# Kernel optimization log

Measured on AMD Instinct MI355X. Metric: run time of the kernel, lower is better.

Reference implementation:

```python
import jax, jax.numpy as jnp
import numpy as np

N_NODES = 20000
N_EDGES = 320000
IN_F = 256
HID = 64
OUT_F = 64
EDGE_F = 16
HEADS = 4
NUM_CLASSES = 10
NUM_GRAPHS = 40
ALPHA = 0.2  # LeakyReLU negative slope


def _xavier(key, shape):
    fan_in, fan_out = shape[0], shape[-1]
    std = 1.414 * np.sqrt(2.0 / (fan_in + fan_out))
    return jax.random.normal(key, shape, dtype=jnp.float32) * std


def setup_inputs() -> dict:
    key = jax.random.key(0)
    ks = jax.random.split(key, 12)
    x = jax.random.normal(ks[0], (N_NODES, IN_F), dtype=jnp.float32)
    edge_index = jax.random.randint(ks[1], (2, N_EDGES), 0, N_NODES, dtype=jnp.int32)
    edge_attr = jax.random.uniform(ks[2], (N_EDGES, EDGE_F), dtype=jnp.float32)
    batch = jnp.sort(jax.random.randint(ks[3], (N_NODES,), 0, NUM_GRAPHS, dtype=jnp.int32))
    # layer 0: in=IN_F, heads=HEADS, out=HID, concat
    W0 = _xavier(ks[4], (IN_F, HEADS * HID))
    a0 = _xavier(ks[5], (HEADS, 2 * HID + EDGE_F))
    # layer 1: in=HID*HEADS, heads=HEADS, out=HID, concat
    W1 = _xavier(ks[6], (HID * HEADS, HEADS * HID))
    a1 = _xavier(ks[7], (HEADS, 2 * HID + EDGE_F))
    # layer 2: in=HID*HEADS, heads=1, out=OUT_F, mean over heads
    W2 = _xavier(ks[8], (HID * HEADS, 1 * OUT_F))
    a2 = _xavier(ks[9], (1, 2 * OUT_F + EDGE_F))
    cls_w = _xavier(ks[10], (OUT_F, NUM_CLASSES))
    cls_b = jnp.zeros((NUM_CLASSES,), dtype=jnp.float32)
    return {"x": x, "edge_index": edge_index, "edge_attr": edge_attr, "batch": batch,
            "W0": W0, "a0": a0, "W1": W1, "a1": a1, "W2": W2, "a2": a2,
            "cls_w": cls_w, "cls_b": cls_b}


def gat_layer(h, W, a, edge_index, edge_attr, heads, out_f, concat):
    n = h.shape[0]
    Wh = (h @ W).reshape(n, heads, out_f)              # [N,H,D]
    src, dst = edge_index[0], edge_index[1]
    a_i, a_j, a_e = a[:, :out_f], a[:, out_f:2 * out_f], a[:, 2 * out_f:]
    # per-node head scores, gathered per edge (equivalent to concat + dot with a)
    s_i = jnp.einsum('nhd,hd->nh', Wh, a_i)            # [N,H]
    s_j = jnp.einsum('nhd,hd->nh', Wh, a_j)            # [N,H]
    s_e = edge_attr @ a_e.T                            # [E,H]
    e = s_i[src] + s_j[dst] + s_e                      # [E,H]
    e = jnp.where(e > 0, e, ALPHA * e)                 # LeakyReLU
    # NB: faithful to source — softmax over the HEADS dim (dim=1), not per-node
    att = jax.nn.softmax(e, axis=1)                    # [E,H]
    msg = att[:, :, None] * Wh[dst]                    # [E,H,D]
    h_prime = jax.ops.segment_sum(msg, src, num_segments=n)  # scatter-add to src
    if concat:
        return jax.nn.elu(h_prime.reshape(n, heads * out_f))
    return h_prime.mean(axis=1)


def reference(x, edge_index, edge_attr, batch, W0, a0, W1, a1, W2, a2, cls_w, cls_b):
    h = gat_layer(x, W0, a0, edge_index, edge_attr, HEADS, HID, True)
    h = gat_layer(h, W1, a1, edge_index, edge_attr, HEADS, HID, True)
    h = gat_layer(h, W2, a2, edge_index, edge_attr, 1, OUT_F, False)
    # global mean pool over graphs
    sums = jax.ops.segment_sum(h, batch, num_segments=NUM_GRAPHS)
    cnts = jax.ops.segment_sum(jnp.ones((h.shape[0],), h.dtype), batch, num_segments=NUM_GRAPHS)
    pooled = sums / jnp.maximum(cnts, 1.0)[:, None]
    logits = pooled @ cls_w + cls_b
    return jax.nn.log_softmax(logits, axis=1)
```

## Files before the change

kernel.cpp:

```cpp
#include <hip/hip_runtime.h>
#include <hip/hip_bf16.h>
#include <math.h>

#define N_NODES 20000
#define N_EDGES 320000
#define IN_F 256
#define HID 64
#define HEADS 4
#define OUT_F 64
#define EDGE_F 16
#define NUM_CLASSES 10
#define NUM_GRAPHS 40
#define LRELU_ALPHA 0.2f

typedef short bf16x8 __attribute__((ext_vector_type(8)));
typedef unsigned short u16x8 __attribute__((ext_vector_type(8)));
typedef float f32x4 __attribute__((ext_vector_type(4)));

static __device__ __forceinline__ float bf2f(unsigned short u) {
    union { unsigned int i; float f; } v; v.i = ((unsigned int)u) << 16; return v.f;
}
static __device__ __forceinline__ unsigned short f2bf(float f) {
    union { float f; unsigned int i; } v; v.f = f;
    unsigned int r = v.i + 0x7FFF + ((v.i >> 16) & 1);
    return (unsigned short)(r >> 16);
}
static __device__ __forceinline__ float eluf(float a) {
    return a > 0.f ? a : __expf(a) - 1.0f;
}

__global__ void prep_kernel(const float* __restrict__ W0, const float* __restrict__ W1,
                            const float* __restrict__ W2, unsigned short* __restrict__ W0b,
                            unsigned short* __restrict__ W1b, unsigned short* __restrict__ W2b,
                            int* __restrict__ cnt) {
    int b = blockIdx.x;
    if (b < 144) {
        int i = b * 256 + threadIdx.x;
        const float* src; unsigned short* dst; int off;
        if (i < 16384)      { src = W0; dst = W0b; off = i; }
        else if (i < 32768) { src = W1; dst = W1b; off = i - 16384; }
        else                { src = W2; dst = W2b; off = i - 32768; }
        float4 v = ((const float4*)src)[off];
        ushort4 o;
        o.x = f2bf(v.x); o.y = f2bf(v.y); o.z = f2bf(v.z); o.w = f2bf(v.w);
        ((ushort4*)dst)[off] = o;
    } else {
        int j = (b - 144) * 256 + threadIdx.x;
        if (j < N_NODES / 4) ((int4*)cnt)[j] = make_int4(0, 0, 0, 0);
    }
}

__global__ void count_kernel(const int4* __restrict__ src4, int* __restrict__ cnt) {
    int i = blockIdx.x * blockDim.x + threadIdx.x;
    if (i < N_EDGES / 4) {
        int4 s = src4[i];
        atomicAdd(&cnt[s.x], 1);
        atomicAdd(&cnt[s.y], 1);
        atomicAdd(&cnt[s.z], 1);
        atomicAdd(&cnt[s.w], 1);
    }
}

__global__ __launch_bounds__(1024) void scan_kernel(const int* __restrict__ cnt,
                                                    int* __restrict__ row_ptr,
                                                    int* __restrict__ cursor) {
    __shared__ int wsum[16];
    __shared__ int carry_s;
    int t = threadIdx.x;
    int lane = t & 63, wave = t >> 6;
    if (t == 0) { carry_s = 0; row_ptr[0] = 0; }
    __syncthreads();
    for (int base = 0; base < N_NODES; base += 1024) {
        int idx = base + t;
        int x0 = (idx < N_NODES) ? cnt[idx] : 0;
        int x = x0;
#pragma unroll
        for (int off = 1; off < 64; off <<= 1) {
            int y = __shfl_up(x, off, 64);
            if (lane >= off) x += y;
        }
        if (lane == 63) wsum[wave] = x;
        __syncthreads();
        if (wave == 0 && lane < 16) {
            int s = wsum[lane];
#pragma unroll
            for (int off = 1; off < 16; off <<= 1) {
                int y = __shfl_up(s, off, 64);
                if (lane >= off) s += y;
            }
            wsum[lane] = s;
        }
        __syncthreads();
        int waveoff = (wave > 0) ? wsum[wave - 1] : 0;
        int carry = carry_s;
        if (idx < N_NODES) {
            int incl = x + waveoff + carry;
            row_ptr[idx + 1] = incl;
            cursor[idx] = incl - x0;
        }
        __syncthreads();
        if (t == 0) carry_s = carry + wsum[15];
        __syncthreads();
    }
}

__global__ void scatter_kernel(const int* __restrict__ src, const int* __restrict__ dst,
                               const float* __restrict__ ea, const float* __restrict__ a0,
                               const float* __restrict__ a1, int* __restrict__ cursor,
                               int* __restrict__ srcp, int* __restrict__ dstp,
                               float* __restrict__ se01) {
    __shared__ float ae[2][4][16];
    int tid = threadIdx.x;
    if (tid < 64) ae[0][tid >> 4][tid & 15] = a0[(tid >> 4) * 144 + 128 + (tid & 15)];
    else if (tid < 128) { int t = tid - 64; ae[1][t >> 4][t & 15] = a1[(t >> 4) * 144 + 128 + (t & 15)]; }
    __syncthreads();
    int e = blockIdx.x * blockDim.x + tid;
    if (e >= N_EDGES) return;
    int s = src[e];
    int pos = atomicAdd(&cursor[s], 1);
    srcp[pos] = s;
    dstp[pos] = dst[e];
    float x[16];
#pragma unroll
    for (int k = 0; k < 16; k += 4) {
        float4 v = *(const float4*)(ea + (size_t)e * 16 + k);
        x[k] = v.x; x[k + 1] = v.y; x[k + 2] = v.z; x[k + 3] = v.w;
    }
    float4 o0 = make_float4(0.f, 0.f, 0.f, 0.f), o1 = o0;
#pragma unroll
    for (int k = 0; k < 16; ++k) {
        o0.x += x[k] * ae[0][0][k]; o0.y += x[k] * ae[0][1][k];
        o0.z += x[k] * ae[0][2][k]; o0.w += x[k] * ae[0][3][k];
        o1.x += x[k] * ae[1][0][k]; o1.y += x[k] * ae[1][1][k];
        o1.z += x[k] * ae[1][2][k]; o1.w += x[k] * ae[1][3][k];
    }
    ((float4*)se01)[(size_t)pos * 2]     = o0;
    ((float4*)se01)[(size_t)pos * 2 + 1] = o1;
}

template <bool AF32, bool SCORES>
__global__ __launch_bounds__(256) void gemm_bf16(const void* __restrict__ Aptr,
                                                 const unsigned short* __restrict__ B,
                                                 unsigned short* __restrict__ C,
                                                 const float* __restrict__ avec,
                                                 float* __restrict__ si, float* __restrict__ sj,
                                                 int M, int N, int K) {
    __shared__ unsigned short As[128][40];
    __shared__ unsigned short Bs[64][40];
    __shared__ unsigned short Cs[128][72];
    __shared__ float sa[128];
    int tid = threadIdx.x;
    if (SCORES && tid < 128) sa[tid] = avec[blockIdx.y * 144 + tid];
    int bm = blockIdx.x * 128, bn = blockIdx.y * 64;
    int w = tid >> 6, l = tid & 63;
    int wr = w * 32;
    int lr = l & 15, lk = (l >> 4) * 8;
    f32x4 acc[2][4] = {};
    int ar = tid >> 1, akc = (tid & 1) * 16;
    int bk = tid >> 3, bn8 = tid & 7, bnc = bn8 * 8;

    for (int k0 = 0; k0 < K; k0 += 32) {
        bf16x8 av0 = {}, av1 = {};
        if (bm + ar < M) {
            if constexpr (AF32) {
                const float* Af = (const float*)Aptr + (size_t)(bm + ar) * K + k0 + akc;
                float4 f0 = ((const float4*)Af)[0];
                float4 f1 = ((const float4*)Af)[1];
                float4 f2 = ((const float4*)Af)[2];
                float4 f3 = ((const float4*)Af)[3];
                av0[0] = (short)f2bf(f0.x); av0[1] = (short)f2bf(f0.y);
                av0[2] = (short)f2bf(f0.z); av0[3] = (short)f2bf(f0.w);
                av0[4] = (short)f2bf(f1.x); av0[5] = (short)f2bf(f1.y);
                av0[6] = (short)f2bf(f1.z); av0[7] = (short)f2bf(f1.w);
                av1[0] = (short)f2bf(f2.x); av1[1] = (short)f2bf(f2.y);
                av1[2] = (short)f2bf(f2.z); av1[3] = (short)f2bf(f2.w);
                av1[4] = (short)f2bf(f3.x); av1[5] = (short)f2bf(f3.y);
                av1[6] = (short)f2bf(f3.z); av1[7] = (short)f2bf(f3.w);
            } else {
                const unsigned short* Ab = (const unsigned short*)Aptr + (size_t)(bm + ar) * K + k0 + akc;
                av0 = *(const bf16x8*)Ab;
                av1 = *(const bf16x8*)(Ab + 8);
            }
        }
        *(bf16x8*)&As[ar][akc] = av0;
        *(bf16x8*)&As[ar][akc + 8] = av1;
        bf16x8 bv = *(const bf16x8*)(B + (size_t)(k0 + bk) * N + bn + bnc);
#pragma unroll
        for (int j = 0; j < 8; ++j) {
            int jj = (j + bn8) & 7;
            Bs[bnc + jj][bk] = (unsigned short)bv[jj];
        }
        __syncthreads();
        bf16x8 a0 = *(const bf16x8*)&As[wr + lr][lk];
        bf16x8 a1 = *(const bf16x8*)&As[wr + 16 + lr][lk];
        bf16x8 b0 = *(const bf16x8*)&Bs[lr][lk];
        bf16x8 b1 = *(const bf16x8*)&Bs[16 + lr][lk];
        bf16x8 b2 = *(const bf16x8*)&Bs[32 + lr][lk];
        bf16x8 b3 = *(const bf16x8*)&Bs[48 + lr][lk];
        acc[0][0] = __builtin_amdgcn_mfma_f32_16x16x32_bf16(a0, b0, acc[0][0], 0, 0, 0);
        acc[0][1] = __builtin_amdgcn_mfma_f32_16x16x32_bf16(a0, b1, acc[0][1], 0, 0, 0);
        acc[0][2] = __builtin_amdgcn_mfma_f32_16x16x32_bf16(a0, b2, acc[0][2], 0, 0, 0);
        acc[0][3] = __builtin_amdgcn_mfma_f32_16x16x32_bf16(a0, b3, acc[0][3], 0, 0, 0);
        acc[1][0] = __builtin_amdgcn_mfma_f32_16x16x32_bf16(a1, b0, acc[1][0], 0, 0, 0);
        acc[1][1] = __builtin_amdgcn_mfma_f32_16x16x32_bf16(a1, b1, acc[1][1], 0, 0, 0);
        acc[1][2] = __builtin_amdgcn_mfma_f32_16x16x32_bf16(a1, b2, acc[1][2], 0, 0, 0);
        acc[1][3] = __builtin_amdgcn_mfma_f32_16x16x32_bf16(a1, b3, acc[1][3], 0, 0, 0);
        __syncthreads();
    }
#pragma unroll
    for (int i = 0; i < 2; ++i)
#pragma unroll
        for (int j = 0; j < 4; ++j)
#pragma unroll
            for (int r = 0; r < 4; ++r)
                Cs[wr + i * 16 + (l >> 4) * 4 + r][j * 16 + (l & 15)] = f2bf(acc[i][j][r]);
    __syncthreads();
    {
        int row = tid >> 3, cc = (tid & 7) * 8;
#pragma unroll
        for (int p = 0; p < 4; ++p, row += 32) {
            if (bm + row < M) {
                bf16x8 o = *(const bf16x8*)&Cs[row][cc];
                *(bf16x8*)(C + (size_t)(bm + row) * N + bn + cc) = o;
            }
        }
    }
    if (SCORES) {
        int r = tid >> 1, half = tid & 1;
        float s0 = 0.f, s1 = 0.f;
#pragma unroll
        for (int k = 0; k < 32; ++k) {
            float f = bf2f(Cs[r][half * 32 + k]);
            s0 += f * sa[half * 32 + k];
            s1 += f * sa[64 + half * 32 + k];
        }
        s0 += __shfl_xor(s0, 1, 64);
        s1 += __shfl_xor(s1, 1, 64);
        if (half == 0 && bm + r < M) {
            si[(size_t)(bm + r) * 4 + blockIdx.y] = s0;
            sj[(size_t)(bm + r) * 4 + blockIdx.y] = s1;
        }
    }
}

__global__ void att_kernel(const int* __restrict__ srcp, const int* __restrict__ dstp,
                           const float4* __restrict__ sev, const float* __restrict__ si,
                           const float* __restrict__ sj, float4* __restrict__ attp) {
    int i = blockIdx.x * blockDim.x + threadIdx.x;
    if (i >= N_EDGES) return;
    int s = srcp[i], u = dstp[i];
    float4 siv = ((const float4*)si)[s];
    float4 sjv = ((const float4*)sj)[u];
    float4 se4 = sev[(size_t)i * 2];
    float t0 = siv.x + sjv.x + se4.x;
    float t1 = siv.y + sjv.y + se4.y;
    float t2 = siv.z + sjv.z + se4.z;
    float t3 = siv.w + sjv.w + se4.w;
    t0 = t0 > 0.f ? t0 : LRELU_ALPHA * t0;
    t1 = t1 > 0.f ? t1 : LRELU_ALPHA * t1;
    t2 = t2 > 0.f ? t2 : LRELU_ALPHA * t2;
    t3 = t3 > 0.f ? t3 : LRELU_ALPHA * t3;
    float m = fmaxf(fmaxf(t0, t1), fmaxf(t2, t3));
    float p0 = __expf(t0 - m), p1 = __expf(t1 - m), p2 = __expf(t2 - m), p3 = __expf(t3 - m);
    float inv = 1.0f / (p0 + p1 + p2 + p3);
    attp[i] = make_float4(p0 * inv, p1 * inv, p2 * inv, p3 * inv);
}

__global__ __launch_bounds__(256) void edge_agg_concat(
    const unsigned short* __restrict__ Whb, const float4* __restrict__ attp,
    const int* __restrict__ row_ptr, const int* __restrict__ dstp,
    unsigned short* __restrict__ out) {
    int v = blockIdx.x * 4 + (threadIdx.x >> 6);
    if (v >= N_NODES) return;
    int l = threadIdx.x & 63;
    int slot = l >> 4, p = l & 15;
    int beg = row_ptr[v], end = row_ptr[v + 1];
    float acc0[8] = {}, acc1[8] = {};
    int i = beg + slot;
    int u_n = 0;
    float4 at_n = make_float4(0.f, 0.f, 0.f, 0.f);
    if (i < end) { u_n = dstp[i]; at_n = attp[i]; }
    for (; i < end; i += 4) {
        int u = u_n;
        float4 at4 = at_n;
        if (i + 4 < end) { u_n = dstp[i + 4]; at_n = attp[i + 4]; }
        const unsigned short* row = Whb + (size_t)u * 256;
        u16x8 w0 = *(const u16x8*)(row + p * 8);
        u16x8 w1 = *(const u16x8*)(row + 128 + p * 8);
        float atA = (p & 8) ? at4.y : at4.x;
        float atB = (p & 8) ? at4.w : at4.z;
#pragma unroll
        for (int j = 0; j < 8; ++j) acc0[j] += atA * bf2f(w0[j]);
#pragma unroll
        for (int j = 0; j < 8; ++j) acc1[j] += atB * bf2f(w1[j]);
    }
#pragma unroll
    for (int j = 0; j < 8; ++j) {
        acc0[j] += __shfl_xor(acc0[j], 16, 64);
        acc0[j] += __shfl_xor(acc0[j], 32, 64);
        acc1[j] += __shfl_xor(acc1[j], 16, 64);
        acc1[j] += __shfl_xor(acc1[j], 32, 64);
    }
    if (slot == 0) {
        u16x8 o0, o1;
#pragma unroll
        for (int j = 0; j < 8; ++j) {
            o0[j] = f2bf(eluf(acc0[j]));
            o1[j] = f2bf(eluf(acc1[j]));
        }
        *(u16x8*)(out + (size_t)v * 256 + p * 8) = o0;
        *(u16x8*)(out + (size_t)v * 256 + 128 + p * 8) = o1;
    }
}

__global__ __launch_bounds__(256) void edge_agg_single(
    const unsigned short* __restrict__ Whb, const int* __restrict__ row_ptr,
    const int* __restrict__ dstp, float* __restrict__ out) {
    int v = blockIdx.x * 4 + (threadIdx.x >> 6);
    if (v >= N_NODES) return;
    int l = threadIdx.x & 63;
    int slot = l >> 3, p = l & 7;
    int beg = row_ptr[v], end = row_ptr[v + 1];
    float acc[8] = {};
    int i = beg + slot;
    int u_n = 0;
    if (i < end) u_n = dstp[i];
    for (; i < end; i += 8) {
        int u = u_n;
        if (i + 8 < end) u_n = dstp[i + 8];
        u16x8 w = *(const u16x8*)(Whb + (size_t)u * 64 + p * 8);
#pragma unroll
        for (int j = 0; j < 8; ++j) acc[j] += bf2f(w[j]);
    }
#pragma unroll
    for (int j = 0; j < 8; ++j) {
        acc[j] += __shfl_xor(acc[j], 8, 64);
        acc[j] += __shfl_xor(acc[j], 16, 64);
        acc[j] += __shfl_xor(acc[j], 32, 64);
    }
    if (l < 8) {
        float4 o0 = make_float4(acc[0], acc[1], acc[2], acc[3]);
        float4 o1 = make_float4(acc[4], acc[5], acc[6], acc[7]);
        *(float4*)(out + (size_t)v * 64 + p * 8) = o0;
        *(float4*)(out + (size_t)v * 64 + p * 8 + 4) = o1;
    }
}

__global__ __launch_bounds__(1024) void pool_kernel(const float* __restrict__ h3,
                                                    const int* __restrict__ batch,
                                                    float* __restrict__ pooled) {
    int g = blockIdx.x;
    int lane = threadIdx.x & 63;
    int wave = threadIdx.x >> 6;
    int lo = 0, hi = N_NODES;
    while (lo < hi) { int mid = (lo + hi) >> 1; if (batch[mid] < g) lo = mid + 1; else hi = mid; }
    int start = lo;
    lo = start; hi = N_NODES;
    while (lo < hi) { int mid = (lo + hi) >> 1; if (batch[mid] < g + 1) lo = mid + 1; else hi = mid; }
    int endi = lo;
    float s = 0.f;
    for (int v = start + wave; v < endi; v += 16) s += h3[(size_t)v * 64 + lane];
    __shared__ float red[16][64];
    red[wave][lane] = s;
    __syncthreads();
    if (wave == 0) {
        float t = red[0][lane];
#pragma unroll
        for (int w = 1; w < 16; ++w) t += red[w][lane];
        float c = (float)((endi - start) > 1 ? (endi - start) : 1);
        pooled[g * 64 + lane] = t / c;
    }
}

__global__ void classify_kernel(const float* __restrict__ pooled, const float* __restrict__ cw,
                                const float* __restrict__ cb, float* __restrict__ out) {
    int g = threadIdx.x;
    if (g >= NUM_GRAPHS) return;
    float lg[NUM_CLASSES];
#pragma unroll
    for (int c = 0; c < NUM_CLASSES; ++c) lg[c] = cb[c];
    for (int d = 0; d < OUT_F; ++d) {
        float p = pooled[g * 64 + d];
#pragma unroll
        for (int c = 0; c < NUM_CLASSES; ++c) lg[c] += p * cw[d * NUM_CLASSES + c];
    }
    float m = lg[0];
#pragma unroll
    for (int c = 1; c < NUM_CLASSES; ++c) m = fmaxf(m, lg[c]);
    float s = 0.f;
#pragma unroll
    for (int c = 0; c < NUM_CLASSES; ++c) s += expf(lg[c] - m);
    float lse = m + logf(s);
#pragma unroll
    for (int c = 0; c < NUM_CLASSES; ++c) out[g * NUM_CLASSES + c] = lg[c] - lse;
}

extern "C" void kernel_launch(void* const* d_in, const int* in_sizes, int n_in,
                              void* d_out, int out_size, void* d_ws, size_t ws_size,
                              hipStream_t stream) {
    const float* x   = (const float*)d_in[0];
    const int*   ei  = (const int*)d_in[1];
    const float* ea  = (const float*)d_in[2];
    const int* batch = (const int*)d_in[3];
    const float* W0  = (const float*)d_in[4];
    const float* a0  = (const float*)d_in[5];
    const float* W1  = (const float*)d_in[6];
    const float* a1  = (const float*)d_in[7];
    const float* W2  = (const float*)d_in[8];
    const float* cw  = (const float*)d_in[10];
    const float* cb  = (const float*)d_in[11];
    float* out = (float*)d_out;

    const int* srcg = ei;
    const int* dstg = ei + N_EDGES;

    char* ws = (char*)d_ws;
    size_t off = 0;
    auto alloc = [&](size_t bytes) -> char* {
        char* p = ws + off;
        off += (bytes + 255) & ~(size_t)255;
        return p;
    };
    unsigned short* W0b  = (unsigned short*)alloc(256 * 256 * 2);
    unsigned short* W1b  = (unsigned short*)alloc(256 * 256 * 2);
    unsigned short* W2b  = (unsigned short*)alloc(256 * 64 * 2);
    unsigned short* Whb  = (unsigned short*)alloc((size_t)N_NODES * 256 * 2);
    unsigned short* hAb  = (unsigned short*)alloc((size_t)N_NODES * 256 * 2);
    unsigned short* hBb  = (unsigned short*)alloc((size_t)N_NODES * 256 * 2);
    unsigned short* Wh2b = (unsigned short*)alloc((size_t)N_NODES * 64 * 2);
    float* si   = (float*)alloc((size_t)N_NODES * HEADS * 4);
    float* sj   = (float*)alloc((size_t)N_NODES * HEADS * 4);
    float* se01 = (float*)alloc((size_t)N_EDGES * 8 * 4);
    float* attp = (float*)alloc((size_t)N_EDGES * HEADS * 4);
    int* row_ptr = (int*)alloc((N_NODES + 1) * 4);
    int* cursor  = (int*)alloc(N_NODES * 4);
    int* cnt  = (int*)alloc(N_NODES * 4);
    int* srcp = (int*)alloc(N_EDGES * 4);
    int* dstp = (int*)alloc(N_EDGES * 4);
    float* h3 = (float*)alloc((size_t)N_NODES * 64 * 4);
    float* pooled = (float*)alloc(NUM_GRAPHS * 64 * 4);

    prep_kernel<<<144 + (N_NODES / 4 + 255) / 256, 256, 0, stream>>>(W0, W1, W2, W0b, W1b, W2b, cnt);

    count_kernel<<<(N_EDGES / 4 + 255) / 256, 256, 0, stream>>>((const int4*)srcg, cnt);
    scan_kernel<<<1, 1024, 0, stream>>>(cnt, row_ptr, cursor);
    scatter_kernel<<<(N_EDGES + 255) / 256, 256, 0, stream>>>(srcg, dstg, ea, a0, a1, cursor,
                                                              srcp, dstp, se01);

    dim3 ggrid((N_NODES + 127) / 128, 4);
    dim3 ggrid2((N_NODES + 127) / 128, 1);
    int atb = (N_EDGES + 255) / 256;
    int agb = (N_NODES + 3) / 4;

    gemm_bf16<true, true><<<ggrid, 256, 0, stream>>>(x, W0b, Whb, a0, si, sj, N_NODES, 256, 256);
    att_kernel<<<atb, 256, 0, stream>>>(srcp, dstp, (const float4*)se01, si, sj, (float4*)attp);
    edge_agg_concat<<<agb, 256, 0, stream>>>(Whb, (const float4*)attp, row_ptr, dstp, hAb);

    gemm_bf16<false, true><<<ggrid, 256, 0, stream>>>(hAb, W1b, Whb, a1, si, sj, N_NODES, 256, 256);
    att_kernel<<<atb, 256, 0, stream>>>(srcp, dstp, (const float4*)se01 + 1, si, sj, (float4*)attp);
    edge_agg_concat<<<agb, 256, 0, stream>>>(Whb, (const float4*)attp, row_ptr, dstp, hBb);

    gemm_bf16<false, false><<<ggrid2, 256, 0, stream>>>(hBb, W2b, Wh2b, nullptr, nullptr, nullptr,
                                                        N_NODES, 64, 256);
    edge_agg_single<<<agb, 256, 0, stream>>>(Wh2b, row_ptr, dstp, h3);

    pool_kernel<<<NUM_GRAPHS, 1024, 0, stream>>>(h3, batch, pooled);
    classify_kernel<<<1, 64, 0, stream>>>(pooled, cw, cb, out);
}
```

Baseline: 205.8 us.

## Recompute edge-attr scores in attention kernel instead of precomputing in scatter

The CSR scatter kernel now only writes destination indices and an edge permutation, no longer computing and scattering per-edge attribute scores. Each attention kernel reads edge_attr in original order, computes the edge score for its layer, and writes the attention result to the permuted CSR position. This removes the scattered se01 buffer and srcp, but reads edge_attr twice and turns the attention write into a scattered store.

```diff
diff --git a/kernel.cpp b/kernel.cpp
--- a/kernel.cpp
+++ b/kernel.cpp
@@ -105,37 +105,15 @@
 }
 
 __global__ void scatter_kernel(const int* __restrict__ src, const int* __restrict__ dst,
-                               const float* __restrict__ ea, const float* __restrict__ a0,
-                               const float* __restrict__ a1, int* __restrict__ cursor,
-                               int* __restrict__ srcp, int* __restrict__ dstp,
-                               float* __restrict__ se01) {
-    __shared__ float ae[2][4][16];
-    int tid = threadIdx.x;
-    if (tid < 64) ae[0][tid >> 4][tid & 15] = a0[(tid >> 4) * 144 + 128 + (tid & 15)];
-    else if (tid < 128) { int t = tid - 64; ae[1][t >> 4][t & 15] = a1[(t >> 4) * 144 + 128 + (t & 15)]; }
-    __syncthreads();
-    int e = blockIdx.x * blockDim.x + tid;
-    if (e >= N_EDGES) return;
-    int s = src[e];
-    int pos = atomicAdd(&cursor[s], 1);
-    srcp[pos] = s;
-    dstp[pos] = dst[e];
-    float x[16];
-#pragma unroll
-    for (int k = 0; k < 16; k += 4) {
-        float4 v = *(const float4*)(ea + (size_t)e * 16 + k);
-        x[k] = v.x; x[k + 1] = v.y; x[k + 2] = v.z; x[k + 3] = v.w;
-    }
-    float4 o0 = make_float4(0.f, 0.f, 0.f, 0.f), o1 = o0;
-#pragma unroll
-    for (int k = 0; k < 16; ++k) {
-        o0.x += x[k] * ae[0][0][k]; o0.y += x[k] * ae[0][1][k];
-        o0.z += x[k] * ae[0][2][k]; o0.w += x[k] * ae[0][3][k];
-        o1.x += x[k] * ae[1][0][k]; o1.y += x[k] * ae[1][1][k];
-        o1.z += x[k] * ae[1][2][k]; o1.w += x[k] * ae[1][3][k];
-    }
-    ((float4*)se01)[(size_t)pos * 2]     = o0;
-    ((float4*)se01)[(size_t)pos * 2 + 1] = o1;
+                               int* __restrict__ cursor, int* __restrict__ dstp,
+                               int* __restrict__ eperm) {
+    int e = blockIdx.x * blockDim.x + threadIdx.x;
+    if (e < N_EDGES) {
+        int s = src[e];
+        int pos = atomicAdd(&cursor[s], 1);
+        dstp[pos] = dst[e];
+        eperm[e] = pos;
+    }
 }
 
 template <bool AF32, bool SCORES>
@@ -243,19 +221,37 @@
     }
 }
 
-__global__ void att_kernel(const int* __restrict__ srcp, const int* __restrict__ dstp,
-                           const float4* __restrict__ sev, const float* __restrict__ si,
-                           const float* __restrict__ sj, float4* __restrict__ attp) {
-    int i = blockIdx.x * blockDim.x + threadIdx.x;
-    if (i >= N_EDGES) return;
-    int s = srcp[i], u = dstp[i];
+__global__ void att_kernel(const int* __restrict__ src, const int* __restrict__ dst,
+                           const float* __restrict__ ea, const float* __restrict__ avec,
+                           const float* __restrict__ si, const float* __restrict__ sj,
+                           const int* __restrict__ eperm, float4* __restrict__ attp) {
+    __shared__ float ae[4][16];
+    int tid = threadIdx.x;
+    if (tid < 64) ae[tid >> 4][tid & 15] = avec[(tid >> 4) * 144 + 128 + (tid & 15)];
+    __syncthreads();
+    int e = blockIdx.x * blockDim.x + tid;
+    if (e >= N_EDGES) return;
+    int s = src[e], u = dst[e];
     float4 siv = ((const float4*)si)[s];
     float4 sjv = ((const float4*)sj)[u];
-    float4 se4 = sev[(size_t)i * 2];
-    float t0 = siv.x + sjv.x + se4.x;
-    float t1 = siv.y + sjv.y + se4.y;
-    float t2 = siv.z + sjv.z + se4.z;
-    float t3 = siv.w + sjv.w + se4.w;
+    float x[16];
+#pragma unroll
+    for (int k = 0; k < 16; k += 4) {
+        float4 v = *(const float4*)(ea + (size_t)e * 16 + k);
+        x[k] = v.x; x[k + 1] = v.y; x[k + 2] = v.z; x[k + 3] = v.w;
+    }
+    float se0 = 0.f, se1 = 0.f, se2 = 0.f, se3 = 0.f;
+#pragma unroll
+    for (int k = 0; k < 16; ++k) {
+        se0 += x[k] * ae[0][k];
+        se1 += x[k] * ae[1][k];
+        se2 += x[k] * ae[2][k];
+        se3 += x[k] * ae[3][k];
+    }
+    float t0 = siv.x + sjv.x + se0;
+    float t1 = siv.y + sjv.y + se1;
+    float t2 = siv.z + sjv.z + se2;
+    float t3 = siv.w + sjv.w + se3;
     t0 = t0 > 0.f ? t0 : LRELU_ALPHA * t0;
     t1 = t1 > 0.f ? t1 : LRELU_ALPHA * t1;
     t2 = t2 > 0.f ? t2 : LRELU_ALPHA * t2;
@@ -263,7 +259,7 @@
     float m = fmaxf(fmaxf(t0, t1), fmaxf(t2, t3));
     float p0 = __expf(t0 - m), p1 = __expf(t1 - m), p2 = __expf(t2 - m), p3 = __expf(t3 - m);
     float inv = 1.0f / (p0 + p1 + p2 + p3);
-    attp[i] = make_float4(p0 * inv, p1 * inv, p2 * inv, p3 * inv);
+    attp[eperm[e]] = make_float4(p0 * inv, p1 * inv, p2 * inv, p3 * inv);
 }
 
 __global__ __launch_bounds__(256) void edge_agg_concat(
@@ -430,13 +426,12 @@
     unsigned short* Wh2b = (unsigned short*)alloc((size_t)N_NODES * 64 * 2);
     float* si   = (float*)alloc((size_t)N_NODES * HEADS * 4);
     float* sj   = (float*)alloc((size_t)N_NODES * HEADS * 4);
-    float* se01 = (float*)alloc((size_t)N_EDGES * 8 * 4);
     float* attp = (float*)alloc((size_t)N_EDGES * HEADS * 4);
     int* row_ptr = (int*)alloc((N_NODES + 1) * 4);
     int* cursor  = (int*)alloc(N_NODES * 4);
     int* cnt  = (int*)alloc(N_NODES * 4);
-    int* srcp = (int*)alloc(N_EDGES * 4);
     int* dstp = (int*)alloc(N_EDGES * 4);
+    int* eperm = (int*)alloc(N_EDGES * 4);
     float* h3 = (float*)alloc((size_t)N_NODES * 64 * 4);
     float* pooled = (float*)alloc(NUM_GRAPHS * 64 * 4);
 
@@ -444,8 +439,7 @@
 
     count_kernel<<<(N_EDGES / 4 + 255) / 256, 256, 0, stream>>>((const int4*)srcg, cnt);
     scan_kernel<<<1, 1024, 0, stream>>>(cnt, row_ptr, cursor);
-    scatter_kernel<<<(N_EDGES + 255) / 256, 256, 0, stream>>>(srcg, dstg, ea, a0, a1, cursor,
-                                                              srcp, dstp, se01);
+    scatter_kernel<<<(N_EDGES + 255) / 256, 256, 0, stream>>>(srcg, dstg, cursor, dstp, eperm);
 
     dim3 ggrid((N_NODES + 127) / 128, 4);
     dim3 ggrid2((N_NODES + 127) / 128, 1);
@@ -453,11 +447,11 @@
     int agb = (N_NODES + 3) / 4;
 
     gemm_bf16<true, true><<<ggrid, 256, 0, stream>>>(x, W0b, Whb, a0, si, sj, N_NODES, 256, 256);
-    att_kernel<<<atb, 256, 0, stream>>>(srcp, dstp, (const float4*)se01, si, sj, (float4*)attp);
+    att_kernel<<<atb, 256, 0, stream>>>(srcg, dstg, ea, a0, si, sj, eperm, (float4*)attp);
     edge_agg_concat<<<agb, 256, 0, stream>>>(Whb, (const float4*)attp, row_ptr, dstp, hAb);
 
     gemm_bf16<false, true><<<ggrid, 256, 0, stream>>>(hAb, W1b, Whb, a1, si, sj, N_NODES, 256, 256);
-    att_kernel<<<atb, 256, 0, stream>>>(srcp, dstp, (const float4*)se01 + 1, si, sj, (float4*)attp);
+    att_kernel<<<atb, 256, 0, stream>>>(srcg, dstg, ea, a1, si, sj, eperm, (float4*)attp);
     edge_agg_concat<<<agb, 256, 0, stream>>>(Whb, (const float4*)attp, row_ptr, dstp, hBb);
 
     gemm_bf16<false, false><<<ggrid2, 256, 0, stream>>>(hBb, W2b, Wh2b, nullptr, nullptr, nullptr,
```

Result: slower. 211.0 us (+2.5%).
